# Kernel tuning notes

Measured on AMD Instinct MI355X. Metric: run time of the kernel, lower is better.

The kernel has to match this reference:

```python
import jax, jax.numpy as jnp
import numpy as np

DIM = 256; HEADS = 4; HD = DIM // HEADS; SCALE = HD ** -0.5
CBS = 4; CSTRIDE = 2; SBS = 4; NSEL = 16; WS = 7
B = 4; H = 64; W = 64


def _unfold(x, bs, stride):
    # x: (B,H,W,C) -> (B, nh*nw, C*bs*bs), flat channel order matches torch F.unfold
    # (index = c*bs*bs + kh*bs + kw)
    b, h, w, c = x.shape
    nh = (h - bs) // stride + 1
    nw = (w - bs) // stride + 1
    cols = [x[:, kh:kh + nh * stride:stride, kw:kw + nw * stride:stride, :]
            for kh in range(bs) for kw in range(bs)]
    p = jnp.stack(cols, axis=-1)  # (B,nh,nw,C,bs*bs)
    return p.reshape(b, nh * nw, c * bs * bs)


def _rel_pos_index(ws):
    coords = np.stack(np.meshgrid(np.arange(ws), np.arange(ws), indexing='ij')).reshape(2, -1)
    rel = (coords[:, :, None] - coords[:, None, :]).transpose(1, 2, 0).copy()
    rel[:, :, 0] += ws - 1
    rel[:, :, 1] += ws - 1
    rel[:, :, 0] *= 2 * ws - 1
    return jnp.asarray(rel.sum(-1))  # (ws*ws, ws*ws) int


def _mlp(x, w1, b1, w2, b2):
    return jax.nn.gelu(x @ w1 + b1, approximate=False) @ w2 + b2


def _window_attn(x, qkv_w, qkv_b, proj_w, proj_b, bias_table):
    b, c, h, w = x.shape
    ws = WS
    ph = (ws - h % ws) % ws
    pw = (ws - w % ws) % ws
    xp = jnp.pad(x, ((0, 0), (0, 0), (0, ph), (0, pw)))
    hp, wp = h + ph, w + pw
    xw = xp.reshape(b, c, hp // ws, ws, wp // ws, ws).transpose(0, 2, 4, 3, 5, 1).reshape(-1, ws * ws, c)
    bw = xw.shape[0]
    qkv = (xw @ qkv_w + qkv_b).reshape(bw, ws * ws, 3, HEADS, HD).transpose(2, 0, 3, 1, 4)
    q, k, v = qkv[0], qkv[1], qkv[2]
    attn = jnp.einsum('bhnd,bhmd->bhnm', q, k) * SCALE
    rpi = _rel_pos_index(ws)
    bias = bias_table[rpi.reshape(-1)].reshape(ws * ws, ws * ws, HEADS).transpose(2, 0, 1)
    attn = jax.nn.softmax(attn + bias[None], axis=-1)
    o = jnp.einsum('bhnm,bhmd->bhnd', attn, v).transpose(0, 2, 1, 3).reshape(bw, ws * ws, c)
    o = o @ proj_w + proj_b
    o = o.reshape(b, hp // ws, wp // ws, ws, ws, c).transpose(0, 5, 1, 3, 2, 4).reshape(b, c, hp, wp)
    return o[:, :, :h, :w]


def _forward(x, qkv_cmp_w, qkv_cmp_b, qkv_slc_w, qkv_slc_b,
             cmpk_w1, cmpk_b1, cmpk_w2, cmpk_b2,
             cmpv_w1, cmpv_b1, cmpv_w2, cmpv_b2, pos_embed,
             win_qkv_w, win_qkv_b, win_proj_w, win_proj_b, win_bias_table,
             proj_cmp_w, proj_cmp_b, proj_slc_w, proj_slc_b,
             gate_w1, gate_b1, gate_w2, gate_b2):
    b, c, h, w = x.shape
    n = h * w
    xs = x.reshape(b, c, n).transpose(0, 2, 1)  # (B,N,C)

    # --- compressed branch ---
    qkv = (xs @ qkv_cmp_w + qkv_cmp_b).reshape(b, n, 3, HEADS, HD).transpose(2, 0, 3, 1, 4)
    q_c, k_c, v_c = qkv[0], qkv[1], qkv[2]  # (B,heads,N,hd)
    k_flat = k_c.transpose(0, 2, 1, 3).reshape(b, n, c)
    v_flat = v_c.transpose(0, 2, 1, 3).reshape(b, n, c)
    fk = _unfold(k_flat.reshape(b, h, w, c), CBS, CSTRIDE)  # (B,nb,C*16)
    fv = _unfold(v_flat.reshape(b, h, w, c), CBS, CSTRIDE)
    nb = fk.shape[1]
    # replicate torch's reshape of the channel-major unfold vector into (bs*bs, dim)
    kpos = (fk.reshape(b, nb, CBS * CBS, c) + pos_embed[None]).reshape(b, nb, CBS * CBS * c)
    k_cmp = _mlp(kpos, cmpk_w1, cmpk_b1, cmpk_w2, cmpk_b2)  # (B,nb,C)
    v_cmp = _mlp(fv, cmpv_w1, cmpv_b1, cmpv_w2, cmpv_b2)
    kch = k_cmp.reshape(b, nb, HEADS, HD).transpose(0, 2, 1, 3)
    vch = v_cmp.reshape(b, nb, HEADS, HD).transpose(0, 2, 1, 3)
    attn_cmp = jax.nn.softmax(jnp.einsum('bhnd,bhmd->bhnm', q_c, kch) * SCALE, axis=-1)
    out_cmp = jnp.einsum('bhnm,bhmd->bhnd', attn_cmp, vch).transpose(0, 2, 1, 3).reshape(b, n, c)
    out_cmp = out_cmp @ proj_cmp_w + proj_cmp_b

    # --- selected branch ---
    qkv2 = (xs @ qkv_slc_w + qkv_slc_b).reshape(b, n, 3, HEADS, HD).transpose(2, 0, 3, 1, 4)
    q_s, k_s, v_s = qkv2[0], qkv2[1], qkv2[2]
    ks_flat = k_s.transpose(0, 2, 1, 3).reshape(b, n, c)
    vs_flat = v_s.transpose(0, 2, 1, 3).reshape(b, n, c)
    imp = attn_cmp.sum(axis=1).mean(axis=1)  # (B, nb)
    ns = min(NSEL, nb)
    _, idx = jax.lax.top_k(imp, ns)
    fkb = _unfold(ks_flat.reshape(b, h, w, c), SBS, SBS)
    fvb = _unfold(vs_flat.reshape(b, h, w, c), SBS, SBS)
    nb2 = fkb.shape[1]
    kb = fkb.reshape(b, nb2, SBS * SBS, c)
    vb = fvb.reshape(b, nb2, SBS * SBS, c)
    idx = jnp.clip(idx, 0, nb2 - 1)
    k_slc = jnp.take_along_axis(kb, idx[:, :, None, None], axis=1).reshape(b, ns * SBS * SBS, c)
    v_slc = jnp.take_along_axis(vb, idx[:, :, None, None], axis=1).reshape(b, ns * SBS * SBS, c)
    ksh = k_slc.reshape(b, -1, HEADS, HD).transpose(0, 2, 1, 3)
    vsh = v_slc.reshape(b, -1, HEADS, HD).transpose(0, 2, 1, 3)
    attn_slc = jax.nn.softmax(jnp.einsum('bhnd,bhmd->bhnm', q_s, ksh) * SCALE, axis=-1)
    out_slc = jnp.einsum('bhnm,bhmd->bhnd', attn_slc, vsh).transpose(0, 2, 1, 3).reshape(b, n, c)
    out_slc = out_slc @ proj_slc_w + proj_slc_b

    # --- window branch ---
    out_win = _window_attn(x, win_qkv_w, win_qkv_b, win_proj_w, win_proj_b, win_bias_table)
    out_win = out_win.reshape(b, c, n).transpose(0, 2, 1)

    # --- gated combination ---
    g = jax.nn.sigmoid(jax.nn.gelu(xs @ gate_w1 + gate_b1, approximate=False) @ gate_w2 + gate_b2)
    out = g[..., 0:1] * out_cmp + g[..., 1:2] * out_slc + g[..., 2:3] * out_win
    return out.transpose(0, 2, 1).reshape(b, c, h, w)


def setup_inputs() -> dict:
    key = jax.random.key(0)
    ks = jax.random.split(key, 16)
    s = 0.02
    d = {
        'x': jax.random.normal(ks[0], (B, DIM, H, W), jnp.float32),
        'qkv_cmp_w': jax.random.normal(ks[1], (DIM, 3 * DIM)) * s,
        'qkv_cmp_b': jnp.zeros((3 * DIM,)),
        'qkv_slc_w': jax.random.normal(ks[2], (DIM, 3 * DIM)) * s,
        'qkv_slc_b': jnp.zeros((3 * DIM,)),
        'cmpk_w1': jax.random.normal(ks[3], (DIM * CBS * CBS, 2 * DIM)) * s,
        'cmpk_b1': jnp.zeros((2 * DIM,)),
        'cmpk_w2': jax.random.normal(ks[4], (2 * DIM, DIM)) * s,
        'cmpk_b2': jnp.zeros((DIM,)),
        'cmpv_w1': jax.random.normal(ks[5], (DIM * CBS * CBS, 2 * DIM)) * s,
        'cmpv_b1': jnp.zeros((2 * DIM,)),
        'cmpv_w2': jax.random.normal(ks[6], (2 * DIM, DIM)) * s,
        'cmpv_b2': jnp.zeros((DIM,)),
        'pos_embed': jax.random.normal(ks[7], (1, CBS * CBS, DIM)) * s,
        'win_qkv_w': jax.random.normal(ks[8], (DIM, 3 * DIM)) * s,
        'win_qkv_b': jnp.zeros((3 * DIM,)),
        'win_proj_w': jax.random.normal(ks[9], (DIM, DIM)) * s,
        'win_proj_b': jnp.zeros((DIM,)),
        'win_bias_table': jax.random.normal(ks[10], ((2 * WS - 1) ** 2, HEADS)) * s,
        'proj_cmp_w': jax.random.normal(ks[11], (DIM, DIM)) * s,
        'proj_cmp_b': jnp.zeros((DIM,)),
        'proj_slc_w': jax.random.normal(ks[12], (DIM, DIM)) * s,
        'proj_slc_b': jnp.zeros((DIM,)),
        'gate_w1': jax.random.normal(ks[13], (DIM, DIM // 4)) * s,
        'gate_b1': jnp.zeros((DIM // 4,)),
        'gate_w2': jax.random.normal(ks[14], (DIM // 4, 3)) * s,
        'gate_b2': jnp.zeros((3,)),
    }
    return d


def reference(x, qkv_cmp_w, qkv_cmp_b, qkv_slc_w, qkv_slc_b,
              cmpk_w1, cmpk_b1, cmpk_w2, cmpk_b2,
              cmpv_w1, cmpv_b1, cmpv_w2, cmpv_b2, pos_embed,
              win_qkv_w, win_qkv_b, win_proj_w, win_proj_b, win_bias_table,
              proj_cmp_w, proj_cmp_b, proj_slc_w, proj_slc_b,
              gate_w1, gate_b1, gate_w2, gate_b2):
    return _forward(x, qkv_cmp_w, qkv_cmp_b, qkv_slc_w, qkv_slc_b,
                    cmpk_w1, cmpk_b1, cmpk_w2, cmpk_b2,
                    cmpv_w1, cmpv_b1, cmpv_w2, cmpv_b2, pos_embed,
                    win_qkv_w, win_qkv_b, win_proj_w, win_proj_b, win_bias_table,
                    proj_cmp_w, proj_cmp_b, proj_slc_w, proj_slc_b,
                    gate_w1, gate_b1, gate_w2, gate_b2)
```

## Files before the change

kernel.cpp:

```cpp
#include <hip/hip_runtime.h>
#include <stdint.h>
#include <stddef.h>


#define DEV __device__ __forceinline__

typedef __attribute__((ext_vector_type(8))) short short8;
typedef __attribute__((ext_vector_type(4))) float f32x4;
typedef unsigned short u16;

DEV u16 f2bf(float f){
    unsigned u = __float_as_uint(f);
    u += 0x7FFFu + ((u>>16)&1u);
    return (u16)(u>>16);
}
DEV float bf2f(u16 u){ return __uint_as_float(((unsigned)u)<<16); }

__global__ void k_xs(const float* __restrict__ x, u16* __restrict__ xh,
                     u16* __restrict__ xl){
    __shared__ float t[32][33];
    int b = blockIdx.z; int c0 = blockIdx.y*32; int n0 = blockIdx.x*32;
    int tx = threadIdx.x, ty = threadIdx.y;
    for(int i=ty;i<32;i+=8)
        t[i][tx] = x[((size_t)(b*256 + c0+i))*4096 + n0 + tx];
    __syncthreads();
    for(int i=ty;i<32;i+=8){
        float v = t[tx][i];
        u16 h = f2bf(v);
        size_t o = ((size_t)(b*4096 + n0+i))*256 + c0 + tx;
        xh[o] = h;
        xl[o] = f2bf(v - bf2f(h));
    }
}

__global__ void k_wt(const float* __restrict__ W, u16* __restrict__ WT,
                     int K, int N){
    __shared__ float t[32][33];
    int k0 = blockIdx.x*32, n0 = blockIdx.y*32;
    int tx = threadIdx.x, ty = threadIdx.y;
    for(int i=ty;i<32;i+=8)
        if(k0+i<K && n0+tx<N) t[i][tx] = W[(size_t)(k0+i)*N + n0+tx];
    __syncthreads();
    for(int i=ty;i<32;i+=8)
        if(n0+i<N && k0+tx<K) WT[(size_t)(n0+i)*K + k0+tx] = f2bf(t[tx][i]);
}

__global__ void k_wt2(const float* __restrict__ W, u16* __restrict__ Hi,
                      u16* __restrict__ Lo, int K, int N){
    __shared__ float t[32][33];
    int k0 = blockIdx.x*32, n0 = blockIdx.y*32;
    int tx = threadIdx.x, ty = threadIdx.y;
    for(int i=ty;i<32;i+=8)
        if(k0+i<K && n0+tx<N) t[i][tx] = W[(size_t)(k0+i)*N + n0+tx];
    __syncthreads();
    for(int i=ty;i<32;i+=8)
        if(n0+i<N && k0+tx<K){
            float v = t[tx][i];
            u16 h = f2bf(v);
            Hi[(size_t)(n0+i)*K + k0+tx] = h;
            Lo[(size_t)(n0+i)*K + k0+tx] = f2bf(v - bf2f(h));
        }
}

__global__ void k_vt(const float* __restrict__ vc, u16* __restrict__ vt,
                     int NK, int ldk){
    __shared__ float t[32][33];
    int b = blockIdx.z; int k0 = blockIdx.x*32; int c0 = blockIdx.y*32;
    int tx = threadIdx.x, ty = threadIdx.y;
    for(int i=ty;i<32;i+=8){
        int k = k0+i;
        t[i][tx] = (k < NK) ? vc[((size_t)(b*NK + k))*256 + c0 + tx] : 0.f;
    }
    __syncthreads();
    for(int i=ty;i<32;i+=8){
        int k = k0+tx;
        if(k < ldk)
            vt[((size_t)(b*256 + c0+i))*ldk + k] = f2bf(t[tx][i]);
    }
}

__global__ __launch_bounds__(256) void k_gemm(
        const float* __restrict__ A, const float* __restrict__ W,
        const float* __restrict__ bias, float* __restrict__ C,
        int M, int K, int Nn, int act)
{
    __shared__ float As[16][68];
    __shared__ float Bs[16][64];
    const int m0 = blockIdx.y*64, n0 = blockIdx.x*64;
    const int t = threadIdx.x, tx = t&15, ty = t>>4;
    float acc[4][4] = {};
    const int am = t>>2;
    const int ak = (t&3)*4;
    const bool arow_ok = (m0+am) < M;

    for(int k0=0;k0<K;k0+=16){
        float4 av = make_float4(0.f,0.f,0.f,0.f);
        if(arow_ok) av = *reinterpret_cast<const float4*>(&A[(size_t)(m0+am)*K + k0 + ak]);
        As[ak+0][am]=av.x; As[ak+1][am]=av.y; As[ak+2][am]=av.z; As[ak+3][am]=av.w;
        {
            int n = t&63, kb = t>>6;
            #pragma unroll
            for(int r=0;r<4;r++){
                int kk = r*4 + kb; float v = 0.f;
                if(n0+n < Nn) v = W[(size_t)(k0+kk)*Nn + n0+n];
                Bs[kk][n] = v;
            }
        }
        __syncthreads();
        #pragma unroll
        for(int kk=0;kk<16;kk++){
            float a0=As[kk][ty*4+0], a1=As[kk][ty*4+1], a2=As[kk][ty*4+2], a3=As[kk][ty*4+3];
            float b0=Bs[kk][tx*4+0], b1=Bs[kk][tx*4+1], b2=Bs[kk][tx*4+2], b3=Bs[kk][tx*4+3];
            acc[0][0]=fmaf(a0,b0,acc[0][0]); acc[0][1]=fmaf(a0,b1,acc[0][1]);
            acc[0][2]=fmaf(a0,b2,acc[0][2]); acc[0][3]=fmaf(a0,b3,acc[0][3]);
            acc[1][0]=fmaf(a1,b0,acc[1][0]); acc[1][1]=fmaf(a1,b1,acc[1][1]);
            acc[1][2]=fmaf(a1,b2,acc[1][2]); acc[1][3]=fmaf(a1,b3,acc[1][3]);
            acc[2][0]=fmaf(a2,b0,acc[2][0]); acc[2][1]=fmaf(a2,b1,acc[2][1]);
            acc[2][2]=fmaf(a2,b2,acc[2][2]); acc[2][3]=fmaf(a2,b3,acc[2][3]);
            acc[3][0]=fmaf(a3,b0,acc[3][0]); acc[3][1]=fmaf(a3,b1,acc[3][1]);
            acc[3][2]=fmaf(a3,b2,acc[3][2]); acc[3][3]=fmaf(a3,b3,acc[3][3]);
        }
        __syncthreads();
    }
    #pragma unroll
    for(int i=0;i<4;i++){
        int m = m0 + ty*4 + i;
        if(m >= M) continue;
        #pragma unroll
        for(int j=0;j<4;j++){
            int n = n0 + tx*4 + j;
            if(n >= Nn) continue;
            float v = acc[i][j] + (bias ? bias[n] : 0.f);
            if(act==1)      v = 0.5f*v*(1.0f + erff(v*0.70710678118654752f));
            else if(act==2) v = 1.0f/(1.0f + expf(-v));
            C[(size_t)m*Nn + n] = v;
        }
    }
}

template<int WM, int WN, int AM, int BMD, int NSPLIT, int OBF>
__global__ __launch_bounds__(256) void k_mgs(
        const float* __restrict__ Af, const u16* __restrict__ Ah,
        const u16* __restrict__ Al,
        const float* __restrict__ Bf, const u16* __restrict__ Bh,
        const u16* __restrict__ Bl,
        const float* __restrict__ bias, float* __restrict__ C,
        u16* __restrict__ Cb, u16* __restrict__ Cb2,
        int M, int N, int K, int lda, int ldb, int ldc, int act, float scale,
        long zsA, long zsB, long zsC)
{
    constexpr int BM = 32*WM, BN = 32*WN;
    constexpr bool SP = (NSPLIT == 3);
    const long zo = (long)blockIdx.z;
    if(AM==0){ Af += zo*zsA; } else { Ah += zo*zsA; if(AM==2) Al += zo*zsA; }
    if(BMD==0){ Bf += zo*zsB; } else { Bh += zo*zsB; if(BMD==2) Bl += zo*zsB; }
    if(OBF) Cb += zo*zsC; else C += zo*zsC;

    __shared__ u16 Ahi[BM*64];
    __shared__ u16 Alo[SP ? BM*64 : 8];
    __shared__ u16 Bhi[BN*64];
    __shared__ u16 Blo[SP ? BN*64 : 8];

    const int m0 = blockIdx.y*BM, n0 = blockIdx.x*BN;
    const int tid = threadIdx.x, lane = tid&63, wv = tid>>6;
    const int wm = (wv>>1)*(16*WM), wn = (wv&1)*(16*WN);
    f32x4 acc[WM][WN] = {};

    constexpr int TPR_A = 256/BM;
    constexpr int CH_A  = 8/TPR_A;
    const int arow = tid / TPR_A;
    const int acol0 = (tid % TPR_A)*(128/TPR_A);
    constexpr int TPR_B = 256/BN;
    constexpr int CH_B  = 8/TPR_B;
    const int brow = tid / TPR_B;
    const int bcol0 = (tid % TPR_B)*(128/TPR_B);

    for(int kt=0; kt<K; kt+=64){
        {
            const bool ok = (m0+arow) < M;
            #pragma unroll
            for(int c=0;c<CH_A;c++){
                int colbyte = acol0 + c*16;
                int e = colbyte>>1;
                const bool lok = ok && (kt + e + 8 <= K);
                short8 h = {}, l = {};
                if(AM==0){
                    float4 v0 = make_float4(0,0,0,0), v1 = v0;
                    if(lok){
                        const float* src = &Af[(size_t)(m0+arow)*lda + kt + e];
                        v0 = *reinterpret_cast<const float4*>(src);
                        v1 = *reinterpret_cast<const float4*>(src+4);
                    }
                    float vv[8] = {v0.x,v0.y,v0.z,v0.w,v1.x,v1.y,v1.z,v1.w};
                    #pragma unroll
                    for(int j=0;j<8;j++){
                        u16 hb = f2bf(vv[j]);
                        h[j] = (short)hb;
                        if(SP) l[j] = (short)f2bf(vv[j] - bf2f(hb));
                    }
                } else {
                    if(lok){
                        h = *reinterpret_cast<const short8*>(Ah + (size_t)(m0+arow)*lda + kt + e);
                        if(SP && AM==2)
                            l = *reinterpret_cast<const short8*>(Al + (size_t)(m0+arow)*lda + kt + e);
                    }
                }
                int byteoff = arow*128 + (colbyte ^ ((arow&7)<<4));
                *reinterpret_cast<short8*>(reinterpret_cast<char*>(Ahi)+byteoff) = h;
                if(SP)
                    *reinterpret_cast<short8*>(reinterpret_cast<char*>(Alo)+byteoff) = l;
            }
        }
        {
            const bool ok = (n0+brow) < N;
            #pragma unroll
            for(int c=0;c<CH_B;c++){
                int colbyte = bcol0 + c*16;
                int e = colbyte>>1;
                const bool lok = ok && (kt + e + 8 <= K);
                short8 h = {}, l = {};
                if(BMD==0){
                    float4 v0 = make_float4(0,0,0,0), v1 = v0;
                    if(lok){
                        const float* src = &Bf[(size_t)(n0+brow)*ldb + kt + e];
                        v0 = *reinterpret_cast<const float4*>(src);
                        v1 = *reinterpret_cast<const float4*>(src+4);
                    }
                    float vv[8] = {v0.x,v0.y,v0.z,v0.w,v1.x,v1.y,v1.z,v1.w};
                    #pragma unroll
                    for(int j=0;j<8;j++){
                        u16 hb = f2bf(vv[j]);
                        h[j] = (short)hb;
                        if(SP) l[j] = (short)f2bf(vv[j] - bf2f(hb));
                    }
                } else {
                    if(lok){
                        h = *reinterpret_cast<const short8*>(Bh + (size_t)(n0+brow)*ldb + kt + e);
                        if(SP && BMD==2)
                            l = *reinterpret_cast<const short8*>(Bl + (size_t)(n0+brow)*ldb + kt + e);
                    }
                }
                int byteoff = brow*128 + (colbyte ^ ((brow&7)<<4));
                *reinterpret_cast<short8*>(reinterpret_cast<char*>(Bhi)+byteoff) = h;
                if(SP)
                    *reinterpret_cast<short8*>(reinterpret_cast<char*>(Blo)+byteoff) = l;
            }
        }
        __syncthreads();
        #pragma unroll
        for(int kb=0;kb<2;kb++){
            short8 ah[WM], al[WM], bh[WN], bl[WN];
            #pragma unroll
            for(int i=0;i<WM;i++){
                int ar = wm + i*16 + (lane&15);
                int ab = ar*128 + (((kb*64) + ((lane>>4)*16)) ^ ((ar&7)<<4));
                ah[i] = *reinterpret_cast<const short8*>(reinterpret_cast<const char*>(Ahi)+ab);
                if(SP)
                    al[i] = *reinterpret_cast<const short8*>(reinterpret_cast<const char*>(Alo)+ab);
            }
            #pragma unroll
            for(int i=0;i<WN;i++){
                int br = wn + i*16 + (lane&15);
                int bb = br*128 + (((kb*64) + ((lane>>4)*16)) ^ ((br&7)<<4));
                bh[i] = *reinterpret_cast<const short8*>(reinterpret_cast<const char*>(Bhi)+bb);
                if(SP)
                    bl[i] = *reinterpret_cast<const short8*>(reinterpret_cast<const char*>(Blo)+bb);
            }
            #pragma unroll
            for(int mi=0;mi<WM;mi++)
                #pragma unroll
                for(int ni=0;ni<WN;ni++){
                    if(SP){
                        acc[mi][ni] = __builtin_amdgcn_mfma_f32_16x16x32_bf16(
                                          al[mi], bh[ni], acc[mi][ni], 0, 0, 0);
                        acc[mi][ni] = __builtin_amdgcn_mfma_f32_16x16x32_bf16(
                                          ah[mi], bl[ni], acc[mi][ni], 0, 0, 0);
                    }
                    acc[mi][ni] = __builtin_amdgcn_mfma_f32_16x16x32_bf16(
                                      ah[mi], bh[ni], acc[mi][ni], 0, 0, 0);
                }
        }
        __syncthreads();
    }
    #pragma unroll
    for(int mi=0;mi<WM;mi++){
        #pragma unroll
        for(int ni=0;ni<WN;ni++){
            int col = n0 + wn + ni*16 + (lane&15);
            if(col >= N) continue;
            int rowb = m0 + wm + mi*16 + ((lane>>4)*4);
            float bv = bias ? bias[col] : 0.f;
            #pragma unroll
            for(int r=0;r<4;r++){
                int m = rowb + r;
                if(m >= M) continue;
                float v = acc[mi][ni][r]*scale + bv;
                if(act==1)      v = 0.5f*v*(1.0f + erff(v*0.70710678118654752f));
                else if(act==2) v = 1.0f/(1.0f + expf(-v));
                if(OBF==2){
                    u16 hb = f2bf(v);
                    Cb [(size_t)m*ldc + col] = hb;
                    Cb2[(size_t)m*ldc + col] = f2bf(v - bf2f(hb));
                } else if(OBF==1){
                    Cb[(size_t)m*ldc + col] = f2bf(v);
                } else {
                    C [(size_t)m*ldc + col] = v;
                }
            }
        }
    }
}

template<int SPLIT, int IMP, int NKR, int NT, int LDV>
__global__ __launch_bounds__(256) void k_fattn(
    const float* __restrict__ Qg, const u16* __restrict__ Khg,
    const u16* __restrict__ Klg, const u16* __restrict__ VTg,
    float* __restrict__ Og, float* __restrict__ impp)
{
    const int qb = blockIdx.x, h = blockIdx.y, b = blockIdx.z;
    const int tid = threadIdx.x, lane = tid&63, wv = tid>>6;
    const int wm = wv*16;
    const int rgrp = lane>>4;
    const int cidx = lane&15;

    __shared__ u16 Qh[64*64];
    __shared__ u16 Ql[SPLIT?64*64:8];
    __shared__ u16 Kh[64*64];
    __shared__ u16 Kl[SPLIT?64*64:8];
    __shared__ u16 Pl[64*64];
    __shared__ u16 Vl[64*64];
    __shared__ float part[4][64];
    __shared__ float colacc[IMP? NT*64 : 8];

    {
        int row = tid>>2;
        int col0 = (tid&3)*32;
        const float* src = &Qg[((size_t)b*4096 + qb*64 + row)*768 + h*64];
        #pragma unroll
        for(int c=0;c<2;c++){
            int colbyte = col0 + c*16;
            int e = colbyte>>1;
            float4 v0 = *reinterpret_cast<const float4*>(src+e);
            float4 v1 = *reinterpret_cast<const float4*>(src+e+4);
            float vv[8]={v0.x,v0.y,v0.z,v0.w,v1.x,v1.y,v1.z,v1.w};
            short8 hh, ll;
            #pragma unroll
            for(int j=0;j<8;j++){
                u16 hb=f2bf(vv[j]); hh[j]=(short)hb;
                if(SPLIT) ll[j]=(short)f2bf(vv[j]-bf2f(hb));
            }
            int byteoff = row*128 + (colbyte ^ ((row&7)<<4));
            *reinterpret_cast<short8*>(reinterpret_cast<char*>(Qh)+byteoff)=hh;
            if(SPLIT)
                *reinterpret_cast<short8*>(reinterpret_cast<char*>(Ql)+byteoff)=ll;
        }
        if(IMP) for(int k=tid;k<NT*64;k+=256) colacc[k]=0.f;
    }

    float m[4], l[4];
    #pragma unroll
    for(int r=0;r<4;r++){ m[r]=-1e30f; l[r]=0.f; }

    for(int t=0;t<NT;t++){
        const int kt = t*64;
        __syncthreads();
        {
            int row = tid>>2;
            int col0 = (tid&3)*32;
            const bool ok = (kt+row) < NKR;
            const u16* srch = &Khg[((size_t)b*NKR + kt + row)*256 + h*64];
            const u16* srcl = SPLIT ? &Klg[((size_t)b*NKR + kt + row)*256 + h*64] : nullptr;
            #pragma unroll
            for(int c=0;c<2;c++){
                int colbyte = col0 + c*16;
                int e = colbyte>>1;
                short8 hh={}, ll={};
                if(ok){
                    hh = *reinterpret_cast<const short8*>(srch+e);
                    if(SPLIT) ll = *reinterpret_cast<const short8*>(srcl+e);
                }
                int byteoff = row*128 + (colbyte ^ ((row&7)<<4));
                *reinterpret_cast<short8*>(reinterpret_cast<char*>(Kh)+byteoff)=hh;
                if(SPLIT)
                    *reinterpret_cast<short8*>(reinterpret_cast<char*>(Kl)+byteoff)=ll;
            }
        }
        __syncthreads();
        f32x4 acc[4] = {};
        #pragma unroll
        for(int kb=0;kb<2;kb++){
            int koff = kb*64 + rgrp*16;
            int ar = wm + cidx;
            int ab = ar*128 + (koff ^ ((ar&7)<<4));
            short8 ah = *reinterpret_cast<const short8*>(reinterpret_cast<const char*>(Qh)+ab);
            short8 al;
            if(SPLIT) al = *reinterpret_cast<const short8*>(reinterpret_cast<const char*>(Ql)+ab);
            #pragma unroll
            for(int ni=0;ni<4;ni++){
                int br = ni*16 + cidx;
                int bb = br*128 + (koff ^ ((br&7)<<4));
                short8 bh = *reinterpret_cast<const short8*>(reinterpret_cast<const char*>(Kh)+bb);
                if(SPLIT){
                    short8 bl = *reinterpret_cast<const short8*>(reinterpret_cast<const char*>(Kl)+bb);
                    acc[ni] = __builtin_amdgcn_mfma_f32_16x16x32_bf16(al, bh, acc[ni], 0,0,0);
                    acc[ni] = __builtin_amdgcn_mfma_f32_16x16x32_bf16(ah, bl, acc[ni], 0,0,0);
                }
                acc[ni] = __builtin_amdgcn_mfma_f32_16x16x32_bf16(ah, bh, acc[ni], 0,0,0);
            }
        }
        #pragma unroll
        for(int r=0;r<4;r++){
            float sv[4];
            float mx = -1e30f;
            #pragma unroll
            for(int ni=0;ni<4;ni++){
                int col = kt + ni*16 + cidx;
                float s = (col < NKR) ? acc[ni][r]*0.125f : -1e30f;
                sv[ni]=s; mx = fmaxf(mx, s);
            }
            mx = fmaxf(mx, __shfl_xor(mx,1));
            mx = fmaxf(mx, __shfl_xor(mx,2));
            mx = fmaxf(mx, __shfl_xor(mx,4));
            mx = fmaxf(mx, __shfl_xor(mx,8));
            float mn = fmaxf(m[r], mx);
            float e = 0.f;
            #pragma unroll
            for(int ni=0;ni<4;ni++) e += __expf(sv[ni]-mn);
            e += __shfl_xor(e,1); e += __shfl_xor(e,2);
            e += __shfl_xor(e,4); e += __shfl_xor(e,8);
            l[r] = l[r]*__expf(m[r]-mn) + e;
            m[r] = mn;
        }
    }
    float inv[4];
    #pragma unroll
    for(int r=0;r<4;r++) inv[r] = 1.f/l[r];

    f32x4 acc_o[4] = {};
    for(int t=0;t<NT;t++){
        const int kt = t*64;
        __syncthreads();
        {
            int row = tid>>2;
            int col0 = (tid&3)*32;
            const bool ok = (kt+row) < NKR;
            const u16* srch = &Khg[((size_t)b*NKR + kt + row)*256 + h*64];
            const u16* srcl = SPLIT ? &Klg[((size_t)b*NKR + kt + row)*256 + h*64] : nullptr;
            #pragma unroll
            for(int c=0;c<2;c++){
                int colbyte = col0 + c*16;
                int e = colbyte>>1;
                short8 hh={}, ll={};
                if(ok){
                    hh = *reinterpret_cast<const short8*>(srch+e);
                    if(SPLIT) ll = *reinterpret_cast<const short8*>(srcl+e);
                }
                int byteoff = row*128 + (colbyte ^ ((row&7)<<4));
                *reinterpret_cast<short8*>(reinterpret_cast<char*>(Kh)+byteoff)=hh;
                if(SPLIT)
                    *reinterpret_cast<short8*>(reinterpret_cast<char*>(Kl)+byteoff)=ll;
            }
        }
        {
            int row = tid>>2;
            int col0 = (tid&3)*32;
            const u16* src = &VTg[((size_t)b*256 + h*64 + row)*LDV + kt];
            #pragma unroll
            for(int c=0;c<2;c++){
                int colbyte = col0 + c*16;
                int e = colbyte>>1;
                short8 hh={};
                if(kt + e + 8 <= LDV)
                    hh = *reinterpret_cast<const short8*>(src + e);
                int byteoff = row*128 + (colbyte ^ ((row&7)<<4));
                *reinterpret_cast<short8*>(reinterpret_cast<char*>(Vl)+byteoff)=hh;
            }
        }
        __syncthreads();
        f32x4 acc[4] = {};
        #pragma unroll
        for(int kb=0;kb<2;kb++){
            int koff = kb*64 + rgrp*16;
            int ar = wm + cidx;
            int ab = ar*128 + (koff ^ ((ar&7)<<4));
            short8 ah = *reinterpret_cast<const short8*>(reinterpret_cast<const char*>(Qh)+ab);
            short8 al;
            if(SPLIT) al = *reinterpret_cast<const short8*>(reinterpret_cast<const char*>(Ql)+ab);
            #pragma unroll
            for(int ni=0;ni<4;ni++){
                int br = ni*16 + cidx;
                int bb = br*128 + (koff ^ ((br&7)<<4));
                short8 bh = *reinterpret_cast<const short8*>(reinterpret_cast<const char*>(Kh)+bb);
                if(SPLIT){
                    short8 bl = *reinterpret_cast<const short8*>(reinterpret_cast<const char*>(Kl)+bb);
                    acc[ni] = __builtin_amdgcn_mfma_f32_16x16x32_bf16(al, bh, acc[ni], 0,0,0);
                    acc[ni] = __builtin_amdgcn_mfma_f32_16x16x32_bf16(ah, bl, acc[ni], 0,0,0);
                }
                acc[ni] = __builtin_amdgcn_mfma_f32_16x16x32_bf16(ah, bh, acc[ni], 0,0,0);
            }
        }
        float cs[4] = {0.f,0.f,0.f,0.f};
        #pragma unroll
        for(int ni=0;ni<4;ni++){
            #pragma unroll
            for(int r=0;r<4;r++){
                int col = kt + ni*16 + cidx;
                float p = 0.f;
                if(col < NKR)
                    p = __expf(acc[ni][r]*0.125f - m[r]) * inv[r];
                int prow = wm + rgrp*4 + r;
                int pcol = ni*16 + cidx;
                int byteoff = prow*128 + ((pcol*2) ^ ((prow&7)<<4));
                *reinterpret_cast<u16*>(reinterpret_cast<char*>(Pl)+byteoff) = f2bf(p);
                if(IMP) cs[ni] += p;
            }
        }
        if(IMP){
            #pragma unroll
            for(int ni=0;ni<4;ni++){
                cs[ni] += __shfl_xor(cs[ni],16);
                cs[ni] += __shfl_xor(cs[ni],32);
            }
            if(rgrp==0){
                #pragma unroll
                for(int ni=0;ni<4;ni++)
                    part[wv][ni*16+cidx] = cs[ni];
            }
        }
        __syncthreads();
        if(IMP && tid < 64)
            colacc[kt+tid] += ((part[0][tid]+part[1][tid])+part[2][tid])+part[3][tid];
        #pragma unroll
        for(int kb=0;kb<2;kb++){
            int koff = kb*64 + rgrp*16;
            int ar = wm + cidx;
            int ab = ar*128 + (koff ^ ((ar&7)<<4));
            short8 pa = *reinterpret_cast<const short8*>(reinterpret_cast<const char*>(Pl)+ab);
            #pragma unroll
            for(int ni=0;ni<4;ni++){
                int br = ni*16 + cidx;
                int bb = br*128 + (koff ^ ((br&7)<<4));
                short8 vb = *reinterpret_cast<const short8*>(reinterpret_cast<const char*>(Vl)+bb);
                acc_o[ni] = __builtin_amdgcn_mfma_f32_16x16x32_bf16(pa, vb, acc_o[ni], 0,0,0);
            }
        }
    }
    __syncthreads();
    #pragma unroll
    for(int ni=0;ni<4;ni++){
        #pragma unroll
        for(int r=0;r<4;r++){
            int q = qb*64 + wm + rgrp*4 + r;
            int d = ni*16 + cidx;
            Og[((size_t)b*4096 + q)*256 + h*64 + d] = acc_o[ni][r];
        }
    }
    if(IMP){
        size_t base = ((size_t)((b*4+h)*64) + qb)*976;
        for(int k=tid; k<NT*64 && k<976; k+=256)
            impp[base+k] = colacc[k];
    }
}

__global__ void k_unfold2(const float* __restrict__ qkv, const float* __restrict__ pos,
                          u16* __restrict__ kh, u16* __restrict__ kl,
                          u16* __restrict__ vv){
    int row = blockIdx.x;
    int b = row / 961, blk = row % 961;
    int bi = blk / 31, bj = blk % 31;
    for(int j = threadIdx.x; j < 4096; j += 256){
        int ch = j >> 4;
        int khh = (j >> 2) & 3, kw = j & 3;
        int n = (bi*2 + khh)*64 + (bj*2 + kw);
        size_t base = ((size_t)(b*4096) + n)*768 + ch;
        float kv = qkv[base + 256] + pos[j];
        float va = qkv[base + 512];
        u16 h = f2bf(kv);
        kh[(size_t)row*4096 + j] = h;
        kl[(size_t)row*4096 + j] = f2bf(kv - bf2f(h));
        vv[(size_t)row*4096 + j] = f2bf(va);
    }
}

__global__ void k_imp_reduce(const float* __restrict__ impp, float* __restrict__ imp){
    __shared__ float part[4][64];
    int b = blockIdx.y;
    int k = blockIdx.x*64 + (threadIdx.x & 63);
    int rr = threadIdx.x >> 6;
    float s = 0.f;
    if(k < 976){
        for(int r=rr; r<256; r+=4)
            s += impp[((size_t)(b*256) + r)*976 + k];
    }
    part[rr][threadIdx.x & 63] = s;
    __syncthreads();
    if(threadIdx.x < 64 && k < 961){
        float t = ((part[0][threadIdx.x] + part[1][threadIdx.x])
                 + part[2][threadIdx.x]) + part[3][threadIdx.x];
        imp[b*961 + k] = t;
    }
}

__global__ __launch_bounds__(256) void k_topk(const float* __restrict__ imp,
                                              int* __restrict__ idx){
    int b = blockIdx.x;
    __shared__ float v[961];
    __shared__ float wvv[4];
    __shared__ int   wvi[4];
    int t = threadIdx.x;
    int lane = t & 63, wid = t >> 6;
    for(int i=t;i<961;i+=256) v[i] = imp[b*961+i];
    __syncthreads();
    for(int it=0; it<16; it++){
        float bv = -1e30f; int bi = 1<<30;
        for(int i=t;i<961;i+=256){
            float val = v[i];
            if(val > bv){ bv=val; bi=i; }
        }
        #pragma unroll
        for(int off=32; off>0; off>>=1){
            float ov = __shfl_xor(bv, off);
            int   oi = __shfl_xor(bi, off);
            if(ov > bv || (ov == bv && oi < bi)){ bv = ov; bi = oi; }
        }
        if(lane==0){ wvv[wid]=bv; wvi[wid]=bi; }
        __syncthreads();
        if(t==0){
            float gb=wvv[0]; int gi=wvi[0];
            #pragma unroll
            for(int w=1;w<4;w++){
                if(wvv[w]>gb || (wvv[w]==gb && wvi[w]<gi)){ gb=wvv[w]; gi=wvi[w]; }
            }
            idx[b*16+it] = gi;
            v[gi] = -1e30f;
        }
        __syncthreads();
    }
}

__global__ void k_gather_sel(const float* __restrict__ qkv2, const int* __restrict__ idx,
                             u16* __restrict__ Ks, float* __restrict__ Vs){
    int row = blockIdx.x;
    int b = row >> 8, tt = row & 255;
    int sel = tt >> 4, p = tt & 15;
    int blk = idx[b*16+sel]; if(blk > 255) blk = 255;
    int bi = blk >> 4, bj = blk & 15;
    int cc = threadIdx.x;
    int y = bi*4 + ((cc>>2)&3), xx = bj*4 + (cc&3);
    int ch = p*16 + (cc>>4);
    size_t src = ((size_t)(b*4096) + y*64 + xx)*768;
    Ks[(size_t)row*256 + cc] = f2bf(qkv2[src + 256 + ch]);
    Vs[(size_t)row*256 + cc] = qkv2[src + 512 + ch];
}

__global__ void k_xw(const u16* __restrict__ xh, u16* __restrict__ xw){
    int row = blockIdx.x;
    int wb = row / 49, t = row % 49;
    int b = wb / 100, wrem = wb % 100;
    int wy = wrem / 10, wx = wrem % 10;
    int ty = t / 7, tx = t % 7;
    int y = wy*7 + ty, xx = wx*7 + tx;
    int c = threadIdx.x;
    u16 v = 0;
    if(y < 64 && xx < 64) v = xh[((size_t)(b*4096) + y*64 + xx)*256 + c];
    xw[(size_t)row*256 + c] = v;
}

__global__ __launch_bounds__(64) void k_attn_win(
    const u16* __restrict__ qkvw, const float* __restrict__ btab,
    u16* __restrict__ outp)
{
    const int wb = blockIdx.x, h = blockIdx.y;
    const int lane = threadIdx.x;
    __shared__ float lk[49][64];
    __shared__ float lv[49][64];
    __shared__ float ls[49][51];
    __shared__ float lbias[169];
    for(int i=lane;i<169;i+=64) lbias[i] = btab[i*4 + h];
    for(int r=0;r<49;r++){
        lk[r][lane] = bf2f(qkvw[((size_t)(wb*49 + r))*768 + 256 + h*64 + lane]);
        lv[r][lane] = bf2f(qkvw[((size_t)(wb*49 + r))*768 + 512 + h*64 + lane]);
    }
    __syncthreads();
    if(lane < 49){
        const u16* qptr = &qkvw[((size_t)(wb*49 + lane))*768 + h*64];
        float qreg[64];
        #pragma unroll
        for(int d=0;d<64;++d) qreg[d] = bf2f(qptr[d]);
        int ih = lane/7, iw = lane%7;
        float m = -1e30f;
        for(int j=0;j<49;j++){
            float s0=0,s1=0,s2=0,s3=0;
            #pragma unroll
            for(int d=0; d<64; d+=4){
                s0 = fmaf(qreg[d+0], lk[j][d+0], s0);
                s1 = fmaf(qreg[d+1], lk[j][d+1], s1);
                s2 = fmaf(qreg[d+2], lk[j][d+2], s2);
                s3 = fmaf(qreg[d+3], lk[j][d+3], s3);
            }
            int jh=j/7, jw=j%7;
            float s = ((s0+s1)+(s2+s3))*0.125f + lbias[(ih-jh+6)*13 + (iw-jw+6)];
            ls[lane][j] = s;
            m = fmaxf(m, s);
        }
        float l = 0.f;
        for(int j=0;j<49;j++){ float p = __expf(ls[lane][j] - m); ls[lane][j] = p; l += p; }
        float inv = 1.f/l;
        u16* op = &outp[((size_t)(wb*49 + lane))*256 + h*64];
        for(int d=0;d<64;d++){
            float a0=0,a1=0;
            for(int j=0;j<48;j+=2){
                a0 = fmaf(ls[lane][j],   lv[j][d],   a0);
                a1 = fmaf(ls[lane][j+1], lv[j+1][d], a1);
            }
            a0 = fmaf(ls[lane][48], lv[48][d], a0);
            op[d] = f2bf((a0+a1)*inv);
        }
    }
}

__global__ void k_combine(const float* __restrict__ ocp, const float* __restrict__ osp,
                          const float* __restrict__ owp, const float* __restrict__ g,
                          float* __restrict__ out){
    __shared__ float tile[32][33];
    int b = blockIdx.z; int c0 = blockIdx.y*32, n0 = blockIdx.x*32;
    int tx = threadIdx.x, ty = threadIdx.y;
    for(int i=ty;i<32;i+=8){
        int n = n0 + i;
        float g0 = g[(size_t)(b*4096+n)*3 + 0];
        float g1 = g[(size_t)(b*4096+n)*3 + 1];
        float g2 = g[(size_t)(b*4096+n)*3 + 2];
        int y = n >> 6, xx = n & 63;
        int wy = y/7, ty2 = y%7, wx = xx/7, tx2 = xx%7;
        size_t wrow = (size_t)(b*100 + wy*10 + wx)*49 + ty2*7 + tx2;
        size_t base = ((size_t)(b*4096) + n)*256 + c0;
        float vc = ocp[base + tx];
        float vs = osp[base + tx];
        float vw = owp[wrow*256 + c0 + tx];
        tile[i][tx] = g0*vc + g1*vs + g2*vw;
    }
    __syncthreads();
    for(int i=ty;i<32;i+=8)
        out[((size_t)(b*256 + c0+i))*4096 + n0 + tx] = tile[tx][i];
}

extern "C" void kernel_launch(void* const* d_in, const int* in_sizes, int n_in,
                              void* d_out, int out_size, void* d_ws, size_t ws_size,
                              hipStream_t stream)
{
    typedef const float* fp;
    fp x          = (fp)d_in[0];
    fp qkv_cmp_w  = (fp)d_in[1];  fp qkv_cmp_b = (fp)d_in[2];
    fp qkv_slc_w  = (fp)d_in[3];  fp qkv_slc_b = (fp)d_in[4];
    fp cmpk_w1    = (fp)d_in[5];  fp cmpk_b1   = (fp)d_in[6];
    fp cmpk_w2    = (fp)d_in[7];  fp cmpk_b2   = (fp)d_in[8];
    fp cmpv_w1    = (fp)d_in[9];  fp cmpv_b1   = (fp)d_in[10];
    fp cmpv_w2    = (fp)d_in[11]; fp cmpv_b2   = (fp)d_in[12];
    fp pos_embed  = (fp)d_in[13];
    fp win_qkv_w  = (fp)d_in[14]; fp win_qkv_b = (fp)d_in[15];
    fp win_proj_w = (fp)d_in[16]; fp win_proj_b= (fp)d_in[17];
    fp win_btab   = (fp)d_in[18];
    fp proj_cmp_w = (fp)d_in[19]; fp proj_cmp_b= (fp)d_in[20];
    fp proj_slc_w = (fp)d_in[21]; fp proj_slc_b= (fp)d_in[22];
    fp gate_w1    = (fp)d_in[23]; fp gate_b1   = (fp)d_in[24];
    fp gate_w2    = (fp)d_in[25]; fp gate_b2   = (fp)d_in[26];
    (void)in_sizes; (void)n_in; (void)out_size;

    char* ws = (char*)d_ws;
    size_t off = 0;
    auto alloc = [&](size_t bytes)->size_t{
        size_t r = off; off += (bytes + 255) & ~(size_t)255; return r;
    };
    const size_t XSH  = alloc((size_t)16384*256*2);
    const size_t XSL  = alloc((size_t)16384*256*2);
    const size_t QKV  = alloc((size_t)16384*768*4);
    const size_t BIGA = alloc((size_t)4*4096*976*4);
    const size_t HID  = alloc((size_t)3844*512*4);
    const size_t KCH  = alloc((size_t)3844*256*2);
    const size_t KCL  = alloc((size_t)3844*256*2);
    const size_t VC   = alloc((size_t)3844*256*4);
    const size_t S_IMPP = (size_t)4096*976*4;
    const size_t S_OC   = (size_t)16384*256*4;
    const size_t S_PB   = (size_t)4*4096*976*2;
    const size_t POOL = alloc(S_IMPP + S_OC + S_OC + S_PB);
    const size_t IMP  = alloc((size_t)4*961*4);
    const size_t IDX  = alloc((size_t)4*16*4);
    const size_t KS   = alloc((size_t)4*256*256*2);
    const size_t VS   = alloc((size_t)4*256*256*4);
    const size_t G2   = alloc((size_t)16384*3*4);
    const size_t VTC  = alloc((size_t)4*256*976*2);
    const size_t VTS  = alloc((size_t)4*256*256*2);
    const size_t TQS  = alloc((size_t)768*256*2);
    const size_t TWQ  = alloc((size_t)768*256*2);
    const size_t TV1  = alloc((size_t)512*4096*2);
    const size_t TV2  = alloc((size_t)256*512*2);
    const size_t TPC  = alloc((size_t)256*256*2);
    const size_t TPS  = alloc((size_t)256*256*2);
    const size_t TWP  = alloc((size_t)256*256*2);
    const size_t TG1  = alloc((size_t)64*256*2);
    const size_t TQCH = alloc((size_t)768*256*2);
    const size_t TQCL = alloc((size_t)768*256*2);
    const size_t TK1H = alloc((size_t)512*4096*2);
    const size_t TK1L = alloc((size_t)512*4096*2);
    const size_t TK2H = alloc((size_t)256*512*2);
    const size_t TK2L = alloc((size_t)256*512*2);
    if(off > ws_size) return;

    u16*   p_xsh = (u16*)(ws + XSH);
    u16*   p_xsl = (u16*)(ws + XSL);
    float* p_qkv = (float*)(ws + QKV);
    u16*   p_bigb= (u16*)  (ws + BIGA);
    u16*   p_uv  = (u16*)  (ws + BIGA);
    float* p_oslc= (float*)(ws + BIGA);
    float* p_owp = (float*)(ws + BIGA + 20971520);
    float* p_hid = (float*)(ws + HID);
    u16*   p_kch = (u16*)(ws + KCH);
    u16*   p_kcl = (u16*)(ws + KCL);
    float* p_vc  = (float*)(ws + VC);
    float* p_impp= (float*)(ws + POOL);
    float* p_oc  = (float*)(ws + POOL + S_IMPP);
    float* p_ocp = (float*)(ws + POOL + S_IMPP + S_OC);
    u16*   p_ukh = (u16*)  (ws + POOL);
    u16*   p_ukl = p_ukh + (size_t)3844*4096;
    u16*   p_xwb = (u16*)  (ws + POOL);
    u16*   p_owin= (u16*)  (ws + POOL + S_IMPP);
    float* p_imp = (float*)(ws + IMP);
    int*   p_idx = (int*)  (ws + IDX);
    u16*   p_ks  = (u16*)(ws + KS);
    float* p_vs  = (float*)(ws + VS);
    float* p_g   = (float*)(ws + G2);
    u16*   p_vtc = (u16*)(ws + VTC);
    u16*   p_vts = (u16*)(ws + VTS);
    u16* t_qs = (u16*)(ws + TQS);
    u16* t_wq = (u16*)(ws + TWQ);
    u16* t_v1 = (u16*)(ws + TV1);
    u16* t_v2 = (u16*)(ws + TV2);
    u16* t_pc = (u16*)(ws + TPC);
    u16* t_ps = (u16*)(ws + TPS);
    u16* t_wp = (u16*)(ws + TWP);
    u16* t_g1 = (u16*)(ws + TG1);
    u16* t_qch= (u16*)(ws + TQCH);
    u16* t_qcl= (u16*)(ws + TQCL);
    u16* t_k1h= (u16*)(ws + TK1H);
    u16* t_k1l= (u16*)(ws + TK1L);
    u16* t_k2h= (u16*)(ws + TK2H);
    u16* t_k2l= (u16*)(ws + TK2L);

    auto wt = [&](fp W, u16* WT, int K, int Nn){
        k_wt<<<dim3((K+31)/32, (Nn+31)/32), dim3(32,8), 0, stream>>>(W, WT, K, Nn);
    };
    auto wt2 = [&](fp W, u16* H, u16* L, int K, int Nn){
        k_wt2<<<dim3((K+31)/32, (Nn+31)/32), dim3(32,8), 0, stream>>>(W, H, L, K, Nn);
    };

    wt(qkv_slc_w, t_qs, 256, 768);
    wt(win_qkv_w, t_wq, 256, 768);
    wt(cmpv_w1,   t_v1, 4096, 512);
    wt(cmpv_w2,   t_v2, 512, 256);
    wt(proj_cmp_w,t_pc, 256, 256);
    wt(proj_slc_w,t_ps, 256, 256);
    wt(win_proj_w,t_wp, 256, 256);
    wt(gate_w1,   t_g1, 256, 64);
    wt2(qkv_cmp_w, t_qch, t_qcl, 256, 768);
    wt2(cmpk_w1,   t_k1h, t_k1l, 4096, 512);
    wt2(cmpk_w2,   t_k2h, t_k2l, 512, 256);

    k_xs<<<dim3(128,8,4), dim3(32,8), 0, stream>>>(x, p_xsh, p_xsl);
    k_mgs<4,4,2,2,3,0><<<dim3(6,128), 256, 0, stream>>>(
        nullptr, p_xsh, p_xsl, nullptr, t_qch, t_qcl, qkv_cmp_b, p_qkv, nullptr, nullptr,
        16384, 768, 256, 256, 256, 768, 0, 1.0f, 0, 0, 0);
    k_unfold2<<<3844, 256, 0, stream>>>(p_qkv, pos_embed, p_ukh, p_ukl, p_uv);
    k_mgs<2,2,2,2,3,0><<<dim3(8,61), 256, 0, stream>>>(
        nullptr, p_ukh, p_ukl, nullptr, t_k1h, t_k1l, cmpk_b1, p_hid, nullptr, nullptr,
        3844, 512, 4096, 4096, 4096, 512, 1, 1.0f, 0, 0, 0);
    k_mgs<2,2,0,2,3,2><<<dim3(4,61), 256, 0, stream>>>(
        p_hid, nullptr, nullptr, nullptr, t_k2h, t_k2l, cmpk_b2, nullptr, p_kch, p_kcl,
        3844, 256, 512, 512, 512, 256, 0, 1.0f, 0, 0, 0);
    k_mgs<2,2,1,1,1,0><<<dim3(8,61), 256, 0, stream>>>(
        nullptr, p_uv, nullptr, nullptr, t_v1, nullptr, cmpv_b1, p_hid, nullptr, nullptr,
        3844, 512, 4096, 4096, 4096, 512, 1, 1.0f, 0, 0, 0);
    k_mgs<2,2,0,1,1,0><<<dim3(4,61), 256, 0, stream>>>(
        p_hid, nullptr, nullptr, nullptr, t_v2, nullptr, cmpv_b2, p_vc, nullptr, nullptr,
        3844, 256, 512, 512, 512, 256, 0, 1.0f, 0, 0, 0);
    k_vt<<<dim3(31,8,4), dim3(32,8), 0, stream>>>(p_vc, p_vtc, 961, 976);
    k_fattn<1,1,961,16,976><<<dim3(64,4,4), 256, 0, stream>>>(
        p_qkv, p_kch, p_kcl, p_vtc, p_oc, p_impp);
    k_imp_reduce<<<dim3(16,4), 256, 0, stream>>>(p_impp, p_imp);
    k_topk<<<4, 256, 0, stream>>>(p_imp, p_idx);
    k_mgs<4,4,0,1,1,0><<<dim3(2,128), 256, 0, stream>>>(
        p_oc, nullptr, nullptr, nullptr, t_pc, nullptr, proj_cmp_b, p_ocp, nullptr, nullptr,
        16384, 256, 256, 256, 256, 256, 0, 1.0f, 0, 0, 0);
    k_mgs<4,4,1,1,1,0><<<dim3(6,128), 256, 0, stream>>>(
        nullptr, p_xsh, nullptr, nullptr, t_qs, nullptr, qkv_slc_b, p_qkv, nullptr, nullptr,
        16384, 768, 256, 256, 256, 768, 0, 1.0f, 0, 0, 0);
    k_xw<<<19600, 256, 0, stream>>>(p_xsh, p_xwb);
    k_mgs<4,4,1,1,1,1><<<dim3(6,154), 256, 0, stream>>>(
        nullptr, p_xwb, nullptr, nullptr, t_wq, nullptr, win_qkv_b, nullptr, p_bigb, nullptr,
        19600, 768, 256, 256, 256, 768, 0, 1.0f, 0, 0, 0);
    k_attn_win<<<dim3(400,4), 64, 0, stream>>>(p_bigb, win_btab, p_owin);
    k_mgs<4,4,1,1,1,0><<<dim3(2,154), 256, 0, stream>>>(
        nullptr, p_owin, nullptr, nullptr, t_wp, nullptr, win_proj_b, p_owp, nullptr, nullptr,
        19600, 256, 256, 256, 256, 256, 0, 1.0f, 0, 0, 0);
    k_gather_sel<<<1024, 256, 0, stream>>>(p_qkv, p_idx, p_ks, p_vs);
    k_vt<<<dim3(8,8,4), dim3(32,8), 0, stream>>>(p_vs, p_vts, 256, 256);
    k_fattn<0,0,256,4,256><<<dim3(64,4,4), 256, 0, stream>>>(
        p_qkv, p_ks, nullptr, p_vts, p_oc, nullptr);
    k_mgs<4,4,0,1,1,0><<<dim3(2,128), 256, 0, stream>>>(
        p_oc, nullptr, nullptr, nullptr, t_ps, nullptr, proj_slc_b, p_oslc, nullptr, nullptr,
        16384, 256, 256, 256, 256, 256, 0, 1.0f, 0, 0, 0);
    k_mgs<2,2,1,1,1,0><<<dim3(1,256), 256, 0, stream>>>(
        nullptr, p_xsh, nullptr, nullptr, t_g1, nullptr, gate_b1, p_hid, nullptr, nullptr,
        16384, 64, 256, 256, 256, 64, 1, 1.0f, 0, 0, 0);
    k_gemm<<<dim3(1,256), 256, 0, stream>>>(p_hid, gate_w2, gate_b2, p_g,
                                            16384, 64, 3, 2);
    k_combine<<<dim3(128,8,4), dim3(32,8), 0, stream>>>(p_ocp, p_oslc, p_owp, p_g,
                                                        (float*)d_out);
}
```

Measured before the change: 856.2 us.

## Swizzle GEMM block order, raise wave priority around MFMA, reuse K-low LDS for V

Adds an optional XCD-aware block remapping to the GEMM kernel and enables it for the two large K=4096 compression MLP GEMMs, to improve L2 locality across the 8 chiplets. Wraps MFMA inner loops in the GEMM and flash-attention kernels with s_setprio to favour waves issuing matrix ops. In the split-precision attention kernel, V is now loaded into the Kl buffer after QK^T instead of a separate LDS array, cutting LDS use to raise occupancy at the cost of an extra barrier. The swizzle assumes the grid size is divisible by 8; 8x61=488 is, so every tile is still visited exactly once.

```diff
diff --git a/kernel.cpp b/kernel.cpp
--- a/kernel.cpp
+++ b/kernel.cpp
@@ -138,7 +138,7 @@
     }
 }
 
-template<int WM, int WN, int AM, int BMD, int NSPLIT, int OBF>
+template<int WM, int WN, int AM, int BMD, int NSPLIT, int OBF, int XSW = 0>
 __global__ __launch_bounds__(256) void k_mgs(
         const float* __restrict__ Af, const u16* __restrict__ Ah,
         const u16* __restrict__ Al,
@@ -161,7 +161,14 @@
     __shared__ u16 Bhi[BN*64];
     __shared__ u16 Blo[SP ? BN*64 : 8];
 
-    const int m0 = blockIdx.y*BM, n0 = blockIdx.x*BN;
+    int bx, by;
+    if(XSW){
+        int flat = blockIdx.y * gridDim.x + blockIdx.x;
+        int chunk = (gridDim.x * gridDim.y) >> 3;
+        int nf = (flat & 7)*chunk + (flat >> 3);
+        bx = nf % gridDim.x; by = nf / gridDim.x;
+    } else { bx = blockIdx.x; by = blockIdx.y; }
+    const int m0 = by*BM, n0 = bx*BN;
     const int tid = threadIdx.x, lane = tid&63, wv = tid>>6;
     const int wm = (wv>>1)*(16*WM), wn = (wv&1)*(16*WN);
     f32x4 acc[WM][WN] = {};
@@ -247,6 +254,7 @@
             }
         }
         __syncthreads();
+        __builtin_amdgcn_s_setprio(1);
         #pragma unroll
         for(int kb=0;kb<2;kb++){
             short8 ah[WM], al[WM], bh[WN], bl[WN];
@@ -280,6 +288,7 @@
                                       ah[mi], bh[ni], acc[mi][ni], 0, 0, 0);
                 }
         }
+        __builtin_amdgcn_s_setprio(0);
         __syncthreads();
     }
     #pragma unroll
@@ -328,9 +337,11 @@
     __shared__ u16 Kh[64*64];
     __shared__ u16 Kl[SPLIT?64*64:8];
     __shared__ u16 Pl[64*64];
-    __shared__ u16 Vl[64*64];
+    __shared__ u16 Vsep[SPLIT?8:64*64];
     __shared__ float part[4][64];
     __shared__ float colacc[IMP? NT*64 : 8];
+
+    u16* Vbuf = SPLIT ? Kl : Vsep;
 
     {
         int row = tid>>2;
@@ -387,6 +398,7 @@
         }
         __syncthreads();
         f32x4 acc[4] = {};
+        __builtin_amdgcn_s_setprio(1);
         #pragma unroll
         for(int kb=0;kb<2;kb++){
             int koff = kb*64 + rgrp*16;
@@ -408,6 +420,7 @@
                 acc[ni] = __builtin_amdgcn_mfma_f32_16x16x32_bf16(ah, bh, acc[ni], 0,0,0);
             }
         }
+        __builtin_amdgcn_s_setprio(0);
         #pragma unroll
         for(int r=0;r<4;r++){
             float sv[4];
@@ -461,7 +474,7 @@
                     *reinterpret_cast<short8*>(reinterpret_cast<char*>(Kl)+byteoff)=ll;
             }
         }
-        {
+        if(!SPLIT){
             int row = tid>>2;
             int col0 = (tid&3)*32;
             const u16* src = &VTg[((size_t)b*256 + h*64 + row)*LDV + kt];
@@ -473,11 +486,12 @@
                 if(kt + e + 8 <= LDV)
                     hh = *reinterpret_cast<const short8*>(src + e);
                 int byteoff = row*128 + (colbyte ^ ((row&7)<<4));
-                *reinterpret_cast<short8*>(reinterpret_cast<char*>(Vl)+byteoff)=hh;
+                *reinterpret_cast<short8*>(reinterpret_cast<char*>(Vsep)+byteoff)=hh;
             }
         }
         __syncthreads();
         f32x4 acc[4] = {};
+        __builtin_amdgcn_s_setprio(1);
         #pragma unroll
         for(int kb=0;kb<2;kb++){
             int koff = kb*64 + rgrp*16;
@@ -499,6 +513,23 @@
                 acc[ni] = __builtin_amdgcn_mfma_f32_16x16x32_bf16(ah, bh, acc[ni], 0,0,0);
             }
         }
+        __builtin_amdgcn_s_setprio(0);
+        if(SPLIT){
+            __syncthreads();
+            int row = tid>>2;
+            int col0 = (tid&3)*32;
+            const u16* src = &VTg[((size_t)b*256 + h*64 + row)*LDV + kt];
+            #pragma unroll
+            for(int c=0;c<2;c++){
+                int colbyte = col0 + c*16;
+                int e = colbyte>>1;
+                short8 hh={};
+                if(kt + e + 8 <= LDV)
+                    hh = *reinterpret_cast<const short8*>(src + e);
+                int byteoff = row*128 + (colbyte ^ ((row&7)<<4));
+                *reinterpret_cast<short8*>(reinterpret_cast<char*>(Kl)+byteoff)=hh;
+            }
+        }
         float cs[4] = {0.f,0.f,0.f,0.f};
         #pragma unroll
         for(int ni=0;ni<4;ni++){
@@ -530,6 +561,7 @@
         __syncthreads();
         if(IMP && tid < 64)
             colacc[kt+tid] += ((part[0][tid]+part[1][tid])+part[2][tid])+part[3][tid];
+        __builtin_amdgcn_s_setprio(1);
         #pragma unroll
         for(int kb=0;kb<2;kb++){
             int koff = kb*64 + rgrp*16;
@@ -540,10 +572,11 @@
             for(int ni=0;ni<4;ni++){
                 int br = ni*16 + cidx;
                 int bb = br*128 + (koff ^ ((br&7)<<4));
-                short8 vb = *reinterpret_cast<const short8*>(reinterpret_cast<const char*>(Vl)+bb);
+                short8 vb = *reinterpret_cast<const short8*>(reinterpret_cast<const char*>(Vbuf)+bb);
                 acc_o[ni] = __builtin_amdgcn_mfma_f32_16x16x32_bf16(pa, vb, acc_o[ni], 0,0,0);
             }
         }
+        __builtin_amdgcn_s_setprio(0);
     }
     __syncthreads();
     #pragma unroll
@@ -870,13 +903,13 @@
         nullptr, p_xsh, p_xsl, nullptr, t_qch, t_qcl, qkv_cmp_b, p_qkv, nullptr, nullptr,
         16384, 768, 256, 256, 256, 768, 0, 1.0f, 0, 0, 0);
     k_unfold2<<<3844, 256, 0, stream>>>(p_qkv, pos_embed, p_ukh, p_ukl, p_uv);
-    k_mgs<2,2,2,2,3,0><<<dim3(8,61), 256, 0, stream>>>(
+    k_mgs<2,2,2,2,3,0,1><<<dim3(8,61), 256, 0, stream>>>(
         nullptr, p_ukh, p_ukl, nullptr, t_k1h, t_k1l, cmpk_b1, p_hid, nullptr, nullptr,
         3844, 512, 4096, 4096, 4096, 512, 1, 1.0f, 0, 0, 0);
     k_mgs<2,2,0,2,3,2><<<dim3(4,61), 256, 0, stream>>>(
         p_hid, nullptr, nullptr, nullptr, t_k2h, t_k2l, cmpk_b2, nullptr, p_kch, p_kcl,
         3844, 256, 512, 512, 512, 256, 0, 1.0f, 0, 0, 0);
-    k_mgs<2,2,1,1,1,0><<<dim3(8,61), 256, 0, stream>>>(
+    k_mgs<2,2,1,1,1,0,1><<<dim3(8,61), 256, 0, stream>>>(
         nullptr, p_uv, nullptr, nullptr, t_v1, nullptr, cmpv_b1, p_hid, nullptr, nullptr,
         3844, 512, 4096, 4096, 4096, 512, 1, 1.0f, 0, 0, 0);
     k_mgs<2,2,0,1,1,0><<<dim3(4,61), 256, 0, stream>>>(
```

Result: no change. 862.3 us (+0.7%).
